# Optimization experiments

Measured on AMD Instinct MI355X. Metric: run time of the kernel, lower is better.

The kernel has to match this reference:

```python
import jax, jax.numpy as jnp
import numpy as np
from jax import lax

SEQ, BATCH, IN, H, L = 2048, 64, 512, 3, 4


def setup_inputs() -> dict:
    key = jax.random.key(0)
    ks = jax.random.split(key, 10)
    s_in = 1.0 / np.sqrt(H)  # torch GRU init scale: U(-1/sqrt(H), 1/sqrt(H))
    u = lambda k, shape: jax.random.uniform(k, shape, jnp.float32, -s_in, s_in)
    return {
        "x": jax.random.normal(ks[0], (SEQ, BATCH, IN), jnp.float32),
        "hxs": jnp.zeros((L, BATCH, H), jnp.float32),
        "w_ih0": u(ks[1], (3 * H, IN)),
        "w_hh0": u(ks[2], (3 * H, H)),
        "b_ih0": u(ks[3], (3 * H,)),
        "b_hh0": u(ks[4], (3 * H,)),
        "w_ih_rest": u(ks[5], (L - 1, 3 * H, H)),
        "w_hh_rest": u(ks[6], (L - 1, 3 * H, H)),
        "b_ih_rest": u(ks[7], (L - 1, 3 * H)),
        "b_hh_rest": u(ks[8], (L - 1, 3 * H)),
    }


def _gru_layer(x_seq, h0, w_ih, w_hh, b_ih, b_hh):
    # Precompute input projections for the whole sequence: (T, B, 3H)
    gx = jnp.einsum("tbi,gi->tbg", x_seq, w_ih) + b_ih

    def step(h, gx_t):
        gh = h @ w_hh.T + b_hh  # (B, 3H)
        rx, zx, nx = jnp.split(gx_t, 3, axis=-1)
        rh, zh, nh = jnp.split(gh, 3, axis=-1)
        r = jax.nn.sigmoid(rx + rh)
        z = jax.nn.sigmoid(zx + zh)
        n = jnp.tanh(nx + r * nh)
        h_new = (1.0 - z) * n + z * h
        return h_new, h_new

    h_last, ys = lax.scan(step, h0, gx)
    return ys, h_last


def reference(x, hxs, w_ih0, w_hh0, b_ih0, b_hh0, w_ih_rest, w_hh_rest, b_ih_rest, b_hh_rest):
    out, h = _gru_layer(x, hxs[0], w_ih0, w_hh0, b_ih0, b_hh0)
    h_finals = [h]
    for l in range(w_ih_rest.shape[0]):  # small fixed layer count
        out, h = _gru_layer(out, hxs[l + 1], w_ih_rest[l], w_hh_rest[l], b_ih_rest[l], b_hh_rest[l])
        h_finals.append(h)
    return out, jnp.stack(h_finals)  # (T, B, H), (L, B, H)
```

## Files before the change

### kernel.cpp

```cpp
#include <hip/hip_runtime.h>
#include <hip/hip_bf16.h>

#define T_SEQ 2048
#define CHUNK 16
#define NCHUNK 129
#define L2E  1.44269504088896340736f
#define L2E2 2.88539008177792681472f

typedef float vf2 __attribute__((ext_vector_type(2)));

template<int CTRL>
__device__ __forceinline__ float dppmov(float v) {
    return __int_as_float(__builtin_amdgcn_update_dpp(
        0, __float_as_int(v), CTRL, 0xF, 0xF, true));
}
template<int CTRL>
__device__ __forceinline__ float dppadd(float v) { return v + dppmov<CTRL>(v); }
__device__ __forceinline__ float swzadd16(float v) {
    return v + __int_as_float(__builtin_amdgcn_ds_swizzle(__float_as_int(v), 0x401F));
}
__device__ __forceinline__ float frcp(float x) { return __builtin_amdgcn_rcpf(x); }
__device__ __forceinline__ float ex2(float x)  { return __builtin_amdgcn_exp2f(x); }
__device__ __forceinline__ vf2 pkfma(vf2 a, float b, vf2 c) {
    vf2 bb = { b, b };
    return __builtin_elementwise_fma(a, bb, c);
}

#define RING_BARRIER() asm volatile("s_waitcnt lgkmcnt(0)\ns_barrier" ::: "memory")

__global__ __launch_bounds__(256) void gx0_kernel(
    const float* __restrict__ x, const float* __restrict__ w,
    const float* __restrict__ bias, float* __restrict__ gx0)
{
    const int lane = threadIdx.x & 63;
    const int gw   = (blockIdx.x * 256 + threadIdx.x) >> 6;

    float4 wA[9], wB[9];
#pragma unroll
    for (int g = 0; g < 9; ++g) {
        const float s = (g < 6) ? L2E : -L2E2;
        float4 a = *(const float4*)&w[g * 512 + lane * 4];
        float4 b = *(const float4*)&w[g * 512 + 256 + lane * 4];
        wA[g] = make_float4(a.x * s, a.y * s, a.z * s, a.w * s);
        wB[g] = make_float4(b.x * s, b.y * s, b.z * s, b.w * s);
    }
    const float bval = (lane < 9) ? bias[lane] * ((lane < 6) ? L2E : -L2E2) : 0.f;

    size_t row0 = (size_t)gw * 16;
    const float4* xp = (const float4*)(x + row0 * 512);
    float4 xa = xp[lane];
    float4 xb = xp[64 + lane];

#pragma unroll 1
    for (int i = 0; i < 16; ++i) {
        float4 na = xa, nb = xb;
        if (i < 15) {
            na = xp[(i + 1) * 128 + lane];
            nb = xp[(i + 1) * 128 + 64 + lane];
        }
        float r[9];
#pragma unroll
        for (int g = 0; g < 9; ++g) {
            float s = xa.x * wA[g].x;
            s = fmaf(xa.y, wA[g].y, s);
            s = fmaf(xa.z, wA[g].z, s);
            s = fmaf(xa.w, wA[g].w, s);
            s = fmaf(xb.x, wB[g].x, s);
            s = fmaf(xb.y, wB[g].y, s);
            s = fmaf(xb.z, wB[g].z, s);
            s = fmaf(xb.w, wB[g].w, s);
            s = dppadd<0xB1>(s);
            s = dppadd<0x4E>(s);
            s = dppadd<0x124>(s);
            s = dppadd<0x128>(s);
            s = swzadd16(s);
            s += __shfl_xor(s, 32, 64);
            r[g] = s;
        }
        float o = r[0];
#pragma unroll
        for (int g = 1; g < 9; ++g) o = (lane == g) ? r[g] : o;
        if (lane < 9) gx0[(row0 + i) * 9 + lane] = o + bval;
        xa = na; xb = nb;
    }
}

__global__ __launch_bounds__(128) void gru_scan(
    const float* __restrict__ gx0,
    const float* __restrict__ hxs,
    const float* __restrict__ w_hh0, const float* __restrict__ b_hh0,
    const float* __restrict__ w_ih_rest, const float* __restrict__ w_hh_rest,
    const float* __restrict__ b_ih_rest, const float* __restrict__ b_hh_rest,
    float* __restrict__ out)
{
    __shared__ float4 gxb[3][CHUNK][64];
    __shared__ float  ring[2][CHUNK][64];
    const int tid  = threadIdx.x;
    const int lane = tid & 63;

    if (tid < 64) {
        const int grp = lane >> 4;
        const int r_  = lane & 15;
        const int l   = r_ >> 2;
        const int j   = r_ & 3;
        const bool jok = (j < 3);
        const bool is0 = (l == 0);
        const int  b   = blockIdx.x * 4 + grp;
        const int  row0 = jok ? j : 0;

        vf2 wi01[3], wh01[3], bh01;
        float wi2[3], wh2[3], bh2;
        {
            float wi[3][3], wh[3][3], bh[3];
            const float sc[3] = {L2E, L2E, -L2E2};
#pragma unroll
            for (int m = 0; m < 3; ++m) {
                const int row = m * 3 + row0;
                if (l == 0) {
                    bh[m] = b_hh0[row] * sc[m];
#pragma unroll
                    for (int k = 0; k < 3; ++k) { wi[m][k] = 0.f; wh[m][k] = w_hh0[row * 3 + k] * sc[m]; }
                } else {
                    float bb = b_hh_rest[(l - 1) * 9 + row];
                    if (m < 2) bb += b_ih_rest[(l - 1) * 9 + row];
                    bh[m] = bb * sc[m];
#pragma unroll
                    for (int k = 0; k < 3; ++k) {
                        wi[m][k] = w_ih_rest[((l - 1) * 9 + row) * 3 + k] * sc[m];
                        wh[m][k] = w_hh_rest[((l - 1) * 9 + row) * 3 + k] * sc[m];
                    }
                }
            }
#pragma unroll
            for (int k = 0; k < 3; ++k) {
                wi01[k] = (vf2){wi[0][k], wi[1][k]};
                wh01[k] = (vf2){wh[0][k], wh[1][k]};
                wi2[k] = wi[2][k]; wh2[k] = wh[2][k];
            }
            bh01 = (vf2){bh[0], bh[1]};
            bh2  = bh[2];
        }
        const float bi2 = is0 ? 0.f : b_ih_rest[(l - 1) * 9 + 6 + row0] * (-L2E2);

        if (!(is0 && jok)) {
            const float4 cv = make_float4(0.f, 0.f, bi2, 0.f);
#pragma unroll
            for (int f = 0; f < 3; ++f)
                for (int st = 0; st < CHUNK; ++st)
                    gxb[f][st][lane] = cv;
        }
        float h = jok ? hxs[(l * 64 + b) * 3 + j] : 0.f;

        RING_BARRIER();

        float4 gp[4];
#pragma unroll
        for (int k = 0; k < 4; ++k) gp[k] = gxb[0][k][lane];

        int bufc = 0;

#define GSTEP(P, MODE, TT)                                                          \
        do {                                                                        \
            float4 cc = gp[(P) & 3];                                                \
            if ((P) < CHUNK - 4) gp[(P) & 3] = gxb[bufc][(P) + 4][lane];            \
            else                 gp[(P) & 3] = gxb[bufn][(P) - (CHUNK - 4)][lane];  \
            float hv0 = dppmov<0x00>(h);                                            \
            float hv1 = dppmov<0x55>(h);                                            \
            float hv2 = dppmov<0xAA>(h);                                            \
            float xv0 = dppmov<0x114>(hv0);                                         \
            float xv1 = dppmov<0x114>(hv1);                                         \
            float xv2 = dppmov<0x114>(hv2);                                         \
            vf2 grz = (vf2){cc.x, cc.y};                                            \
            grz = pkfma(wi01[0], xv0, grz);                                         \
            grz = pkfma(wi01[1], xv1, grz);                                         \
            grz = pkfma(wi01[2], xv2, grz);                                         \
            vf2 ghrz = bh01;                                                        \
            ghrz = pkfma(wh01[0], hv0, ghrz);                                       \
            ghrz = pkfma(wh01[1], hv1, ghrz);                                       \
            ghrz = pkfma(wh01[2], hv2, ghrz);                                       \
            vf2 arz = grz + ghrz;                                                   \
            float gxn = fmaf(wi2[0], xv0, fmaf(wi2[1], xv1, fmaf(wi2[2], xv2, cc.z))); \
            float ghn = fmaf(wh2[0], hv0, fmaf(wh2[1], hv1, fmaf(wh2[2], hv2, bh2))); \
            float er = ex2(-arz.x);                                                 \
            float ez = ex2(-fmaxf(arz.y, -60.f));                                   \
            float rr = frcp(1.0f + er);                                             \
            float argn = fminf(fmaf(rr, ghn, gxn), 60.f);                           \
            float en = ex2(argn);                                                   \
            float N  = fmaf(en, h - ez, h + ez);                                    \
            float en1 = en + 1.0f;                                                  \
            float D  = fmaf(en1, ez, en1);                                          \
            float hn = N * frcp(D);                                                 \
            if (MODE == 0)      h = ((TT) >= 0)    ? hn : h;                        \
            else if (MODE == 2) h = ((TT) < T_SEQ) ? hn : h;                        \
            else                h = hn;                                             \
            ring[CB][(P)][lane] = hn;                                               \
        } while (0)

        {
            const int bufn = 1; const int CB = 0;
#pragma unroll
            for (int p = 0; p < 4; ++p)  GSTEP(p, 0, p - l);
#pragma unroll
            for (int p = 4; p < 16; ++p) GSTEP(p, 1, 0);
            RING_BARRIER();
            bufc = 1;
        }
#pragma unroll 1
        for (int c = 1; c < 128; ++c) {
            const int bufn = (bufc == 2) ? 0 : bufc + 1;
            const int CB = c & 1;
#pragma unroll
            for (int p = 0; p < 16; ++p) GSTEP(p, 1, 0);
            RING_BARRIER();
            bufc = bufn;
        }
        {
            const int bufn = (bufc == 2) ? 0 : bufc + 1;
            const int CB = 0;
#pragma unroll
            for (int p = 0; p < 4; ++p) GSTEP(p, 2, 2048 + p - l);
            RING_BARRIER();
        }
#undef GSTEP
        if (jok) out[(size_t)T_SEQ * 192 + (l * 64 + b) * 3 + j] = h;
    } else {
        const int blk = blockIdx.x;
        float* gxs = (float*)gxb;

#define FILL(F, T0)                                                                 \
        do {                                                                        \
            _Pragma("unroll")                                                       \
            for (int k = 0; k < 9; ++k) {                                           \
                int i  = k * 64 + lane;                                             \
                int st = i / 36;                                                    \
                int pos = i - st * 36;                                              \
                int bl = pos / 9;                                                   \
                int g  = pos - bl * 9;                                              \
                int m  = g / 3;                                                     \
                int jj = g - m * 3;                                                 \
                float val = gx0[(size_t)((T0) + st) * 576 + (blk * 4 + bl) * 9 + g];\
                gxs[(((F) * CHUNK + st) * 64 + bl * 16 + jj) * 4 + m] = val;        \
            }                                                                       \
        } while (0)

#define DRAIN(CC)                                                                   \
        do {                                                                        \
            _Pragma("unroll")                                                       \
            for (int k = 0; k < 3; ++k) {                                           \
                int i  = k * 64 + lane;                                             \
                int p  = i / 12;                                                    \
                int q  = i - p * 12;                                                \
                int g2 = q / 3;                                                     \
                int jj = q - g2 * 3;                                                \
                int t  = (CC) * CHUNK + p - 3;                                      \
                float val = ring[(CC) & 1][p][g2 * 16 + 12 + jj];                   \
                if (t >= 0 && t < T_SEQ)                                            \
                    out[(size_t)t * 192 + (blk * 4 + g2) * 3 + jj] = val;           \
            }                                                                       \
        } while (0)

        FILL(0, 0);
        FILL(1, CHUNK);
        RING_BARRIER();

#pragma unroll 1
        for (int c = 0; c < NCHUNK; ++c) {
            const int f = c + 2;
            if (f <= 127) FILL(f % 3, f * CHUNK);
            if (c >= 1)   DRAIN(c - 1);
            RING_BARRIER();
        }
        DRAIN(NCHUNK - 1);
#undef FILL
#undef DRAIN
    }
}

extern "C" void kernel_launch(void* const* d_in, const int* in_sizes, int n_in,
                              void* d_out, int out_size, void* d_ws, size_t ws_size,
                              hipStream_t stream) {
    const float* x         = (const float*)d_in[0];
    const float* hxs       = (const float*)d_in[1];
    const float* w_ih0     = (const float*)d_in[2];
    const float* w_hh0     = (const float*)d_in[3];
    const float* b_ih0     = (const float*)d_in[4];
    const float* b_hh0     = (const float*)d_in[5];
    const float* w_ih_rest = (const float*)d_in[6];
    const float* w_hh_rest = (const float*)d_in[7];
    const float* b_ih_rest = (const float*)d_in[8];
    const float* b_hh_rest = (const float*)d_in[9];
    float* out = (float*)d_out;
    float* gx0 = (float*)d_ws;

    hipLaunchKernelGGL(gx0_kernel, dim3(2048), dim3(256), 0, stream,
                       x, w_ih0, b_ih0, gx0);
    hipLaunchKernelGGL(gru_scan, dim3(16), dim3(128), 0, stream,
                       gx0, hxs, w_hh0, b_hh0, w_ih_rest, w_hh_rest,
                       b_ih_rest, b_hh_rest, out);
}
```

Measured before the change: 223.3 us.

## Split gx LDS buffer into swizzled scalar planes and rebalance GRU step FMAs

Measured after the change: 227.3 us. About the same (+1.8%).

```diff
diff --git a/kernel.cpp b/kernel.cpp
--- a/kernel.cpp
+++ b/kernel.cpp
@@ -80,7 +80,7 @@
         float o = r[0];
 #pragma unroll
         for (int g = 1; g < 9; ++g) o = (lane == g) ? r[g] : o;
-        if (lane < 9) gx0[(row0 + i) * 9 + lane] = o + bval;
+        if (lane < 9) gx0[(row0 + i) * 9 + lane] = fminf(fmaxf(o + bval, -50.f), 50.f);
         xa = na; xb = nb;
     }
 }
@@ -93,12 +93,13 @@
     const float* __restrict__ b_ih_rest, const float* __restrict__ b_hh_rest,
     float* __restrict__ out)
 {
-    __shared__ float4 gxb[3][CHUNK][64];
-    __shared__ float  ring[2][CHUNK][64];
+    __shared__ float gxf[3 * CHUNK * 3 * 64];
+    __shared__ float ring[2][CHUNK][64];
     const int tid  = threadIdx.x;
     const int lane = tid & 63;
 
     if (tid < 64) {
+        __builtin_amdgcn_s_setprio(1);
         const int grp = lane >> 4;
         const int r_  = lane & 15;
         const int l   = r_ >> 2;
@@ -108,6 +109,10 @@
         const int  b   = blockIdx.x * 4 + grp;
         const int  row0 = jok ? j : 0;
 
+        int lx[4];
+#pragma unroll
+        for (int q = 0; q < 4; ++q) lx[q] = lane ^ (q << 2);
+
         vf2 wi01[3], wh01[3], bh01;
         float wi2[3], wh2[3], bh2;
         {
@@ -143,52 +148,62 @@
         const float bi2 = is0 ? 0.f : b_ih_rest[(l - 1) * 9 + 6 + row0] * (-L2E2);
 
         if (!(is0 && jok)) {
-            const float4 cv = make_float4(0.f, 0.f, bi2, 0.f);
+            const float cm[3] = {0.f, 0.f, bi2};
 #pragma unroll
             for (int f = 0; f < 3; ++f)
                 for (int st = 0; st < CHUNK; ++st)
-                    gxb[f][st][lane] = cv;
+#pragma unroll
+                    for (int m = 0; m < 3; ++m)
+                        gxf[((f * CHUNK + st) * 3 + m) * 64 + lx[(st * 3 + m) & 3]] = cm[m];
         }
         float h = jok ? hxs[(l * 64 + b) * 3 + j] : 0.f;
 
         RING_BARRIER();
 
-        float4 gp[4];
-#pragma unroll
-        for (int k = 0; k < 4; ++k) gp[k] = gxb[0][k][lane];
+        float gp[4][3];
+#define PREF(SL, BUF, ST)                                                           \
+        do {                                                                        \
+            const float* _r = gxf + ((BUF) * CHUNK + (ST)) * 192;                   \
+            gp[SL][0] = _r[lx[((ST) * 3 + 0) & 3]];                                 \
+            gp[SL][1] = _r[64 + lx[((ST) * 3 + 1) & 3]];                            \
+            gp[SL][2] = _r[128 + lx[((ST) * 3 + 2) & 3]];                           \
+        } while (0)
+
+#pragma unroll
+        for (int k = 0; k < 4; ++k) PREF(k, 0, k);
 
         int bufc = 0;
 
 #define GSTEP(P, MODE, TT)                                                          \
         do {                                                                        \
-            float4 cc = gp[(P) & 3];                                                \
-            if ((P) < CHUNK - 4) gp[(P) & 3] = gxb[bufc][(P) + 4][lane];            \
-            else                 gp[(P) & 3] = gxb[bufn][(P) - (CHUNK - 4)][lane];  \
+            float c0 = gp[(P) & 3][0], c1 = gp[(P) & 3][1], c2 = gp[(P) & 3][2];    \
+            if ((P) < CHUNK - 4) PREF((P) & 3, bufc, (P) + 4);                      \
+            else                 PREF((P) & 3, bufn, (P) - (CHUNK - 4));            \
             float hv0 = dppmov<0x00>(h);                                            \
             float hv1 = dppmov<0x55>(h);                                            \
             float hv2 = dppmov<0xAA>(h);                                            \
             float xv0 = dppmov<0x114>(hv0);                                         \
             float xv1 = dppmov<0x114>(hv1);                                         \
             float xv2 = dppmov<0x114>(hv2);                                         \
-            vf2 grz = (vf2){cc.x, cc.y};                                            \
-            grz = pkfma(wi01[0], xv0, grz);                                         \
-            grz = pkfma(wi01[1], xv1, grz);                                         \
-            grz = pkfma(wi01[2], xv2, grz);                                         \
-            vf2 ghrz = bh01;                                                        \
-            ghrz = pkfma(wh01[0], hv0, ghrz);                                       \
-            ghrz = pkfma(wh01[1], hv1, ghrz);                                       \
-            ghrz = pkfma(wh01[2], hv2, ghrz);                                       \
-            vf2 arz = grz + ghrz;                                                   \
-            float gxn = fmaf(wi2[0], xv0, fmaf(wi2[1], xv1, fmaf(wi2[2], xv2, cc.z))); \
+            vf2 t1 = pkfma(wh01[0], hv0, bh01);                                     \
+            vf2 t2 = pkfma(wh01[1], hv1, (vf2){c0, c1});                            \
+            t1 = pkfma(wh01[2], hv2, t1);                                           \
+            t2 = pkfma(wi01[0], xv0, t2);                                           \
+            t1 = pkfma(wi01[1], xv1, t1);                                           \
+            t2 = pkfma(wi01[2], xv2, t2);                                           \
+            vf2 arz = t1 + t2;                                                      \
             float ghn = fmaf(wh2[0], hv0, fmaf(wh2[1], hv1, fmaf(wh2[2], hv2, bh2))); \
+            float gxn = fmaf(wi2[0], xv0, fmaf(wi2[1], xv1, fmaf(wi2[2], xv2, c2))); \
             float er = ex2(-arz.x);                                                 \
-            float ez = ex2(-fmaxf(arz.y, -60.f));                                   \
+            float ez = ex2(-arz.y);                                                 \
             float rr = frcp(1.0f + er);                                             \
-            float argn = fminf(fmaf(rr, ghn, gxn), 60.f);                           \
+            float argn = fmaf(rr, ghn, gxn);                                        \
             float en = ex2(argn);                                                   \
-            float N  = fmaf(en, h - ez, h + ez);                                    \
-            float en1 = en + 1.0f;                                                  \
-            float D  = fmaf(en1, ez, en1);                                          \
+            float hm = h - ez;                                                      \
+            float hp = h + ez;                                                      \
+            float N  = fmaf(en, hm, hp);                                            \
+            float enp1 = en + 1.0f;                                                 \
+            float D  = fmaf(enp1, ez, enp1);                                        \
             float hn = N * frcp(D);                                                 \
             if (MODE == 0)      h = ((TT) >= 0)    ? hn : h;                        \
             else if (MODE == 2) h = ((TT) < T_SEQ) ? hn : h;                        \
@@ -222,24 +237,25 @@
             RING_BARRIER();
         }
 #undef GSTEP
+#undef PREF
         if (jok) out[(size_t)T_SEQ * 192 + (l * 64 + b) * 3 + j] = h;
     } else {
         const int blk = blockIdx.x;
-        float* gxs = (float*)gxb;
 
 #define FILL(F, T0)                                                                 \
         do {                                                                        \
             _Pragma("unroll")                                                       \
             for (int k = 0; k < 9; ++k) {                                           \
-                int i  = k * 64 + lane;                                             \
-                int st = i / 36;                                                    \
-                int pos = i - st * 36;                                              \
-                int bl = pos / 9;                                                   \
-                int g  = pos - bl * 9;                                              \
-                int m  = g / 3;                                                     \
-                int jj = g - m * 3;                                                 \
-                float val = gx0[(size_t)((T0) + st) * 576 + (blk * 4 + bl) * 9 + g];\
-                gxs[(((F) * CHUNK + st) * 64 + bl * 16 + jj) * 4 + m] = val;        \
+                int i   = k * 64 + lane;                                            \
+                int st  = i / 36;                                                   \
+                int rem = i - st * 36;                                              \
+                int m   = rem / 12;                                                 \
+                int pos = rem - m * 12;                                             \
+                int bl  = pos / 3;                                                  \
+                int jj  = pos - bl * 3;                                             \
+                float val = gx0[(size_t)((T0) + st) * 576 + (blk * 4 + bl) * 9 + m * 3 + jj]; \
+                int slot = (bl * 16 + jj) ^ ((((st * 3 + m) & 3)) << 2);            \
+                gxf[(((F) * CHUNK + st) * 3 + m) * 64 + slot] = val;                \
             }                                                                       \
         } while (0)
 
```
